# Kernel optimization log

Hardware: AMD Instinct MI355X
Metric: run time of the kernel (lower is better)

Reference implementation:

```python
import jax, jax.numpy as jnp
import numpy as np

N_HIDDEN = 96
N_LAYER = 4
IN_FEAT = 24


def _lstm_layer(xs, W_ih, W_hh, b):
    # xs: [T, B, in]; W_ih: [4H, in]; W_hh: [4H, H]; b: [4H]
    B = xs.shape[1]
    h0 = jnp.zeros((B, N_HIDDEN), xs.dtype)
    c0 = jnp.zeros((B, N_HIDDEN), xs.dtype)

    def step(carry, x_t):
        h, c = carry
        gates = x_t @ W_ih.T + h @ W_hh.T + b  # [B, 4H], torch gate order i,f,g,o
        i, f, g, o = jnp.split(gates, 4, axis=-1)
        i = jax.nn.sigmoid(i)
        f = jax.nn.sigmoid(f)
        g = jnp.tanh(g)
        o = jax.nn.sigmoid(o)
        c = f * c + i * g
        h = o * jnp.tanh(c)
        return (h, c), h

    (hT, cT), ys = jax.lax.scan(step, (h0, c0), xs)
    return ys, hT


def setup_inputs() -> dict:
    key = jax.random.key(0)
    ks = jax.random.split(key, 16)
    B, T = 4096, 128
    k = 1.0 / np.sqrt(N_HIDDEN)  # torch default LSTM init bound
    u = lambda kk, shape: jax.random.uniform(kk, shape, jnp.float32, -k, k)
    inp = {
        "x": jax.random.normal(ks[0], (B, T, IN_FEAT), jnp.float32),
        "W_ih0": u(ks[1], (4 * N_HIDDEN, IN_FEAT)),          # layer 0 input weights
        "W_ih_rest": u(ks[2], (N_LAYER - 1, 4 * N_HIDDEN, N_HIDDEN)),  # layers 1..3
        "W_hh": u(ks[3], (N_LAYER, 4 * N_HIDDEN, N_HIDDEN)),
        "b_ih": u(ks[4], (N_LAYER, 4 * N_HIDDEN)),
        "b_hh": u(ks[5], (N_LAYER, 4 * N_HIDDEN)),
        "fc1_w": u(ks[6], (16, N_HIDDEN)),
        "fc1_b": u(ks[7], (16,)),
        "fc2_w": u(ks[8], (8, 16)),
        "fc2_b": u(ks[9], (8,)),
        "fc3_w": u(ks[10], (1, 8)),
        "fc3_b": u(ks[11], (1,)),
    }
    return inp


def reference(x, W_ih0, W_ih_rest, W_hh, b_ih, b_hh,
              fc1_w, fc1_b, fc2_w, fc2_b, fc3_w, fc3_b):
    # x: [B, T, F] (batch_first); scan over time -> [T, B, F]
    xs = jnp.transpose(x, (1, 0, 2))
    hns = []
    ys, h = _lstm_layer(xs, W_ih0, W_hh[0], b_ih[0] + b_hh[0])
    hns.append(h)
    for l in range(N_LAYER - 1):  # inter-layer dropout p=0.1 -> identity in eval
        ys, h = _lstm_layer(ys, W_ih_rest[l], W_hh[l + 1], b_ih[l + 1] + b_hh[l + 1])
        hns.append(h)
    # original forward detaches hn via numpy round-trip -> stop_gradient
    hn_sum = jax.lax.stop_gradient(hns[-1] + hns[1])  # [B, H]
    z = jax.nn.relu(hn_sum)
    z = jax.nn.relu(z @ fc1_w.T + fc1_b)
    z = jax.nn.relu(z @ fc2_w.T + fc2_b)
    out = z @ fc3_w.T + fc3_b  # head dropout p=0.1 -> identity in eval
    return out  # [B, 1]
```

## Files before the change

kernel.cpp:

```cpp
#include <hip/hip_runtime.h>
#include <math.h>

typedef _Float16 f16;
typedef _Float16 f16x8 __attribute__((ext_vector_type(8)));
typedef float f32x4 __attribute__((ext_vector_type(4)));
typedef float f32x2 __attribute__((ext_vector_type(2)));

#define B_TOTAL 4096
#define T_STEPS 128
#define H 96
#define NB 16
#define NTH 768
#define NBLK (B_TOTAL/NB)
#define GUP 97
#define ST_T (NB*H)

__device__ __forceinline__ float sigf(float v){
    return __builtin_amdgcn_rcpf(1.f + __expf(-v));
}
__device__ __forceinline__ float tanhf_(float v){
    return 1.f - 2.f*__builtin_amdgcn_rcpf(__expf(2.f*v) + 1.f);
}

__device__ __forceinline__ void lds_barrier(){
    __builtin_amdgcn_sched_barrier(0);
    asm volatile("s_waitcnt lgkmcnt(0)" ::: "memory");
    __builtin_amdgcn_s_barrier();
    __builtin_amdgcn_sched_barrier(0);
}

template<int F, bool IS_L0, bool HAS_YSOUT, bool WRITE_HSUM, bool ADD_HSUM>
__device__ __forceinline__ void layer_run(
    const float* __restrict__ x32, f16* __restrict__ strip,
    const float* __restrict__ Wi, const float* __restrict__ Wh,
    const float* __restrict__ bi, const float* __restrict__ bh,
    f16* sh, f16* sl, float* gbuf, float* hsum, int row0)
{
    constexpr int  KS   = (F + H + 31)/32;
    constexpr int  KP   = KS*32;
    constexpr int  KPB  = KP*2;
    constexpr bool HAS_LO = IS_L0;
    constexpr int  BUF  = 16*KP;

    const int tid=threadIdx.x, lane=tid&63, w=tid>>6;
    const int j15=lane&15, g4=lane>>4;
    const int g=w>>1, q0=(w&1)*2;
    const int u=16*g+j15;
    const int eu=tid>>3, er0=(tid&7)*2;
    const int sr=tid/48, su=(tid-sr*48)*2;
    const int ysrd_off = sr*KPB + (((F+su)*2) ^ ((sr&7)<<4));

    for (int i=tid;i<2*BUF;i+=NTH) sh[i]=(f16)0.f;
    if constexpr (HAS_LO)
        for (int i=tid;i<2*BUF;i+=NTH) sl[i]=(f16)0.f;

    f16x8 Bf[2][KS];
#pragma unroll
    for (int qq=0;qq<2;++qq){
        const int j=96*(q0+qq)+u;
#pragma unroll
        for (int s=0;s<KS;++s){
            f16x8 f;
#pragma unroll
            for (int e=0;e<8;++e){
                int k=32*s+8*g4+e;
                float v=0.f;
                if (k<F)        v=Wi[(size_t)j*F+k];
                else if (k-F<H) v=Wh[(size_t)j*H+(k-F)];
                f[e]=(f16)v;
            }
            Bf[qq][s]=f;
        }
    }
    float bq[2];
#pragma unroll
    for (int qq=0;qq<2;++qq) bq[qq]=bi[96*(q0+qq)+u]+bh[96*(q0+qq)+u];

    float c2[2]={0.f,0.f};

    unsigned*       ysst = (unsigned*)strip + tid;
    const unsigned* yld  = (const unsigned*)strip + (ST_T/2) + tid;
    const int yr=(tid*2)/H, yk=(tid*2)-yr*H;
    const int yoff = yr*KPB + ((yk*2)^((yr&7)<<4));

    const int xr=tid/24, xk=tid-xr*24;
    const bool xact = IS_L0 && (tid < NB*24);
    const float* xbase = xact ? x32 + (size_t)(row0+xr)*(T_STEPS*24) + xk : nullptr;
    const int xoff = xr*KPB + ((xk*2)^((xr&7)<<4));

    if constexpr (IS_L0){
        if (xact){
            float v=xbase[0];
            f16 vh=(f16)v, vl=(f16)(v-(float)vh);
            *(f16*)((char*)sh+xoff)=vh; *(f16*)((char*)sl+xoff)=vl;
        }
    } else {
        unsigned v = *((const unsigned*)strip + tid);
        *(unsigned*)((char*)sh+yoff)=v;
    }
    __syncthreads();

    unsigned yvA=0u;
    if constexpr (!IS_L0){ yvA = *yld; yld += ST_T/2; }

    const int aswz=(j15&7)<<4;
    const int abase=j15*KPB;
    int gw[4];
#pragma unroll
    for (int r=0;r<4;++r) gw[r]=(((4*g4+r)*GUP+u)*4+q0)*4;
    int grd[2], nho[2];
#pragma unroll
    for (int s2=0;s2<2;++s2){
        grd[s2]=((er0+s2)*GUP+eu)*16;
        nho[s2]=(er0+s2)*KPB + (((F+eu)*2)^(((er0+s2)&7)<<4));
    }

#pragma unroll 1
    for (int t=0;t<T_STEPS;++t){
        const int cur=t&1, nxt=cur^1;
        const char* chb=(const char*)(sh+cur*BUF);
        const char* clb=HAS_LO ? (const char*)(sl+cur*BUF) : nullptr;
        char*       nhb=(char*)(sh+nxt*BUF);
        char*       nlb=HAS_LO ? (char*)(sl+nxt*BUF) : nullptr;

        float xv=0.f; unsigned yvB=0u;
        if constexpr (IS_L0){
            if (xact && t+1<T_STEPS) xv = xbase[(size_t)(t+1)*24];
        } else {
            if (t+2<T_STEPS){ yvB = *yld; yld += ST_T/2; }
        }
        __builtin_amdgcn_sched_barrier(0);

        unsigned hbits=0u;
        if (HAS_YSOUT && t>0) hbits = *(const unsigned*)(chb + ysrd_off);

        f32x4 acc[2][2];
#pragma unroll
        for (int qq=0;qq<2;++qq){
            f32x4 a={bq[qq],bq[qq],bq[qq],bq[qq]}; acc[qq][0]=a;
            f32x4 z={0.f,0.f,0.f,0.f};              acc[qq][1]=z;
        }
#pragma unroll
        for (int s=0;s<KS;++s){
            int kb=((s*64+g4*16)^aswz);
            f16x8 ah=*(const f16x8*)(chb+abase+kb);
            if (s&1){
                acc[0][1]=__builtin_amdgcn_mfma_f32_16x16x32_f16(ah,Bf[0][s],acc[0][1],0,0,0);
                acc[1][1]=__builtin_amdgcn_mfma_f32_16x16x32_f16(ah,Bf[1][s],acc[1][1],0,0,0);
            } else {
                acc[0][0]=__builtin_amdgcn_mfma_f32_16x16x32_f16(ah,Bf[0][s],acc[0][0],0,0,0);
                acc[1][0]=__builtin_amdgcn_mfma_f32_16x16x32_f16(ah,Bf[1][s],acc[1][0],0,0,0);
            }
        }
        if constexpr (HAS_LO){
            int kb=((g4*16)^aswz);
            f16x8 al=*(const f16x8*)(clb+abase+kb);
            acc[0][1]=__builtin_amdgcn_mfma_f32_16x16x32_f16(al,Bf[0][0],acc[0][1],0,0,0);
            acc[1][1]=__builtin_amdgcn_mfma_f32_16x16x32_f16(al,Bf[1][0],acc[1][1],0,0,0);
        }
#pragma unroll
        for (int r=0;r<4;++r){
            f32x2 p={acc[0][0][r]+acc[0][1][r], acc[1][0][r]+acc[1][1][r]};
            *(f32x2*)((char*)gbuf + gw[r]) = p;
        }
        lds_barrier();

        if (HAS_YSOUT && t>0){ *ysst = hbits; ysst += ST_T/2; }

#pragma unroll
        for (int s2=0;s2<2;++s2){
            f32x4 gv4 = *(const f32x4*)((const char*)gbuf + grd[s2]);
            float iv=sigf(gv4[0]), fv=sigf(gv4[1]);
            float gg=tanhf_(gv4[2]), ov=sigf(gv4[3]);
            float c=fv*c2[s2]+iv*gg;
            c2[s2]=c;
            float h=ov*tanhf_(c);
            *(f16*)(nhb + nho[s2]) = (f16)h;
            if constexpr (WRITE_HSUM){ if (t==T_STEPS-1) hsum[(er0+s2)*96+eu]=h; }
            if constexpr (ADD_HSUM)  { if (t==T_STEPS-1) hsum[(er0+s2)*96+eu]+=h; }
        }
        if (t+1<T_STEPS){
            if constexpr (IS_L0){
                if (xact){
                    f16 vh=(f16)xv, vl=(f16)(xv-(float)vh);
                    *(f16*)(nhb+xoff)=vh; *(f16*)(nlb+xoff)=vl;
                }
            } else {
                *(unsigned*)(nhb+yoff)=yvA;
            }
        }
        lds_barrier();
        yvA = yvB;
    }
    if constexpr (HAS_YSOUT){
        unsigned hbits = *(const unsigned*)((const char*)sh + ysrd_off);
        asm volatile("s_waitcnt lgkmcnt(0)" ::: "memory");
        *ysst = hbits;
    }
}

__global__ __launch_bounds__(NTH, 1)
void lstm_all(const float* __restrict__ x,
              const float* __restrict__ W_ih0,
              const float* __restrict__ W_ih_rest,
              const float* __restrict__ W_hh,
              const float* __restrict__ b_ih,
              const float* __restrict__ b_hh,
              const float* __restrict__ fc1_w, const float* __restrict__ fc1_b,
              const float* __restrict__ fc2_w, const float* __restrict__ fc2_b,
              const float* __restrict__ fc3_w, const float* __restrict__ fc3_b,
              f16* __restrict__ ws_strip, float* __restrict__ out)
{
    __shared__ f16 sh[2*16*192];
    __shared__ f16 sl[2*16*128];
    __shared__ float gbuf[16*GUP*4];
    __shared__ float hsum[16*96];
    __shared__ float z1[16*16];
    __shared__ float z2[16*8];

    const int tid=threadIdx.x;
    const int b=blockIdx.x, row0=b*NB;
    f16* strip = ws_strip + (size_t)b*T_STEPS*ST_T;
    const int GH = 384*96;

    layer_run<24, true,  true,  false, false>(x, strip, W_ih0,             W_hh,        b_ih,          b_hh,          sh,sl,gbuf,hsum,row0);
    __syncthreads();
    layer_run<96, false, true,  true,  false>(nullptr, strip, W_ih_rest,        W_hh+1*GH, b_ih+1*384, b_hh+1*384, sh,sl,gbuf,hsum,row0);
    __syncthreads();
    layer_run<96, false, true,  false, false>(nullptr, strip, W_ih_rest+1*GH, W_hh+2*GH, b_ih+2*384, b_hh+2*384, sh,sl,gbuf,hsum,row0);
    __syncthreads();
    layer_run<96, false, false, false, true >(nullptr, strip, W_ih_rest+2*GH, W_hh+3*GH, b_ih+3*384, b_hh+3*384, sh,sl,gbuf,hsum,row0);
    __syncthreads();

    if (tid<256){
        int r=tid>>4, jj=tid&15;
        float a=fc1_b[jj];
        for (int uu=0;uu<96;++uu) a+=fc1_w[jj*96+uu]*fmaxf(hsum[r*96+uu],0.f);
        z1[r*16+jj]=fmaxf(a,0.f);
    }
    __syncthreads();
    if (tid<128){
        int r=tid>>3, jj=tid&7;
        float a=fc2_b[jj];
#pragma unroll
        for (int uu=0;uu<16;++uu) a+=fc2_w[jj*16+uu]*z1[r*16+uu];
        z2[r*8+jj]=fmaxf(a,0.f);
    }
    __syncthreads();
    if (tid<16){
        float a=fc3_b[0];
#pragma unroll
        for (int uu=0;uu<8;++uu) a+=fc3_w[uu]*z2[tid*8+uu];
        out[row0+tid]=a;
    }
}

extern "C" void kernel_launch(void* const* d_in, const int* in_sizes, int n_in,
                              void* d_out, int out_size, void* d_ws, size_t ws_size,
                              hipStream_t stream) {
    const float* x         = (const float*)d_in[0];
    const float* W_ih0     = (const float*)d_in[1];
    const float* W_ih_rest = (const float*)d_in[2];
    const float* W_hh      = (const float*)d_in[3];
    const float* b_ih      = (const float*)d_in[4];
    const float* b_hh      = (const float*)d_in[5];
    const float* fc1_w     = (const float*)d_in[6];
    const float* fc1_b     = (const float*)d_in[7];
    const float* fc2_w     = (const float*)d_in[8];
    const float* fc2_b     = (const float*)d_in[9];
    const float* fc3_w     = (const float*)d_in[10];
    const float* fc3_b     = (const float*)d_in[11];
    float* out = (float*)d_out;

    const size_t WS = (size_t)NBLK * T_STEPS * ST_T * sizeof(f16);
    if (ws_size < WS) {
        hipMemsetAsync(d_out, 0, (size_t)out_size * sizeof(float), stream);
        return;
    }

    lstm_all<<<dim3(NBLK), dim3(NTH), 0, stream>>>(
        x, W_ih0, W_ih_rest, W_hh, b_ih, b_hh,
        fc1_w, fc1_b, fc2_w, fc2_b, fc3_w, fc3_b,
        (f16*)d_ws, out);
}
```

Baseline: 612.7 us.

## Fold log2e scaling into weights and apply gate activations in MFMA epilogue

```diff
diff --git a/kernel.cpp b/kernel.cpp
--- a/kernel.cpp
+++ b/kernel.cpp
@@ -14,12 +14,16 @@
 #define NBLK (B_TOTAL/NB)
 #define GUP 97
 #define ST_T (NB*H)
-
-__device__ __forceinline__ float sigf(float v){
-    return __builtin_amdgcn_rcpf(1.f + __expf(-v));
-}
-__device__ __forceinline__ float tanhf_(float v){
-    return 1.f - 2.f*__builtin_amdgcn_rcpf(__expf(2.f*v) + 1.f);
+#define LOG2E 1.44269504088896f
+
+__device__ __forceinline__ float sig2(float vp){
+    return __builtin_amdgcn_rcpf(1.f + __builtin_amdgcn_exp2f(-vp));
+}
+__device__ __forceinline__ float tanh2(float vpp){
+    return 1.f - 2.f*__builtin_amdgcn_rcpf(__builtin_amdgcn_exp2f(vpp) + 1.f);
+}
+__device__ __forceinline__ float tanh_c(float c){
+    return tanh2(c * (2.f*LOG2E));
 }
 
 __device__ __forceinline__ void lds_barrier(){
@@ -55,6 +59,9 @@
         for (int i=tid;i<2*BUF;i+=NTH) sl[i]=(f16)0.f;
 
     f16x8 Bf[2][KS];
+    float scl[2];
+#pragma unroll
+    for (int qq=0;qq<2;++qq) scl[qq] = (q0+qq==2) ? 2.f*LOG2E : LOG2E;
 #pragma unroll
     for (int qq=0;qq<2;++qq){
         const int j=96*(q0+qq)+u;
@@ -67,14 +74,15 @@
                 float v=0.f;
                 if (k<F)        v=Wi[(size_t)j*F+k];
                 else if (k-F<H) v=Wh[(size_t)j*H+(k-F)];
-                f[e]=(f16)v;
+                f[e]=(f16)(v*scl[qq]);
             }
             Bf[qq][s]=f;
         }
     }
     float bq[2];
 #pragma unroll
-    for (int qq=0;qq<2;++qq) bq[qq]=bi[96*(q0+qq)+u]+bh[96*(q0+qq)+u];
+    for (int qq=0;qq<2;++qq)
+        bq[qq]=(bi[96*(q0+qq)+u]+bh[96*(q0+qq)+u])*scl[qq];
 
     float c2[2]={0.f,0.f};
 
@@ -160,7 +168,11 @@
         }
 #pragma unroll
         for (int r=0;r<4;++r){
-            f32x2 p={acc[0][0][r]+acc[0][1][r], acc[1][0][r]+acc[1][1][r]};
+            float v0=acc[0][0][r]+acc[0][1][r];
+            float v1=acc[1][0][r]+acc[1][1][r];
+            float a0 = (q0==0) ? sig2(v0) : tanh2(v0);
+            float a1 = sig2(v1);
+            f32x2 p={a0,a1};
             *(f32x2*)((char*)gbuf + gw[r]) = p;
         }
         lds_barrier();
@@ -170,11 +182,9 @@
 #pragma unroll
         for (int s2=0;s2<2;++s2){
             f32x4 gv4 = *(const f32x4*)((const char*)gbuf + grd[s2]);
-            float iv=sigf(gv4[0]), fv=sigf(gv4[1]);
-            float gg=tanhf_(gv4[2]), ov=sigf(gv4[3]);
-            float c=fv*c2[s2]+iv*gg;
+            float c = gv4[1]*c2[s2] + gv4[0]*gv4[2];
             c2[s2]=c;
-            float h=ov*tanhf_(c);
+            float h = gv4[3]*tanh_c(c);
             *(f16*)(nhb + nho[s2]) = (f16)h;
             if constexpr (WRITE_HSUM){ if (t==T_STEPS-1) hsum[(er0+s2)*96+eu]=h; }
             if constexpr (ADD_HSUM)  { if (t==T_STEPS-1) hsum[(er0+s2)*96+eu]+=h; }
```

New measurement: 581.8 us. 5.0% less time.
